# Optimization experiments

Measured on AMD Instinct MI355X. Metric: run time of the kernel, lower is better.

## Reference

```python
import jax, jax.numpy as jnp
import numpy as np

HOPS = 3
VOCAB, EMBD, STORY_LEN, SENT_LEN, BATCH, QLEN = 50000, 128, 200, 32, 64, 32
INIT_RNG = 0.1


def setup_inputs() -> dict:
    key = jax.random.key(0)
    k1, k2, k3, k4, k5 = jax.random.split(key, 5)
    x = jax.random.randint(k1, (BATCH, STORY_LEN, SENT_LEN), 0, VOCAB)          # story token ids
    q = jax.random.randint(k2, (BATCH, QLEN), 0, VOCAB)                          # question token ids
    # hops+1 embedding tables, initialized ~ Normal(mean=-0.1, std=0.1) as in the torch code
    A = jax.random.normal(k3, (HOPS + 1, VOCAB, EMBD), dtype=jnp.float32) * INIT_RNG - INIT_RNG
    TA = jax.random.normal(k4, (STORY_LEN,), dtype=jnp.float32) * INIT_RNG - INIT_RNG
    TC = jax.random.normal(k5, (STORY_LEN,), dtype=jnp.float32) * INIT_RNG - INIT_RNG
    return {"A": A, "TA": TA, "TC": TC, "x": x, "q": q}


def reference(A, TA, TC, x, q):
    # dropout p=0.0 -> identity
    # u: question embedding, summed over query tokens -> [B, E]
    u = jnp.take(A[1], q, axis=0).sum(axis=1)
    for k in range(HOPS):
        # memory (m) and output (c) representations: gather + sum over sentence tokens + temporal encoding
        m = jnp.take(A[k], x, axis=0).sum(axis=2) + TA[None, :, None]      # [B, S, E]
        c = jnp.take(A[k + 1], x, axis=0).sum(axis=2) + TC[None, :, None]  # [B, S, E]
        p = jax.nn.softmax(jnp.einsum("bse,be->bs", m, u), axis=-1)        # attention over story [B, S]
        u = jnp.einsum("bse,bs->be", c, p) + u                              # weighted combine + residual
    logits = u @ A[HOPS].T                                                  # W = A[-1].weight.T -> [B, V]
    return jax.nn.log_softmax(logits, axis=-1)
```

## Files before the change

### kernel.cpp

```cpp
#include <hip/hip_runtime.h>
#include <math.h>

#define VOCAB 50000
#define EMBD  128
#define SLEN  200
#define TOK   32
#define BATCH 64
#define QLEN  32
#define NSENT (BATCH*SLEN)
#define NTASK (4*NSENT + BATCH)
#define TBL   ((size_t)VOCAB*EMBD)
#define NTILE 3125

typedef short short8 __attribute__((ext_vector_type(8)));
typedef float f32x4  __attribute__((ext_vector_type(4)));

__device__ inline float bits2f(unsigned u){ union{unsigned u; float f;}c; c.u=u; return c.f; }
__device__ inline unsigned f2bits(float f){ union{float f; unsigned u;}c; c.f=f; return c.u; }
__device__ inline unsigned pack_bf16(float lo, float hi){
    unsigned ul = f2bits(lo), uh = f2bits(hi);
    unsigned rl = (ul + 0x7fffu + ((ul>>16)&1u)) >> 16;
    unsigned rh = (uh + 0x7fffu + ((uh>>16)&1u)) >> 16;
    return rl | (rh<<16);
}
__device__ inline unsigned short bf16of(float f){
    unsigned u = f2bits(f);
    return (unsigned short)((u + 0x7fffu + ((u>>16)&1u)) >> 16);
}

__device__ inline float waveSum(float v) {
    #pragma unroll
    for (int o = 32; o > 0; o >>= 1) v += __shfl_down(v, o, 64);
    return v;
}
__device__ inline float waveMax(float v) {
    #pragma unroll
    for (int o = 32; o > 0; o >>= 1) v = fmaxf(v, __shfl_down(v, o, 64));
    return v;
}

__global__ __launch_bounds__(256) void conv_kernel(
    const float* __restrict__ A, unsigned* __restrict__ Ab)
{
    size_t i = ((size_t)blockIdx.x*256 + threadIdx.x)*8;
    float4 a = *(const float4*)(A+i);
    float4 b = *(const float4*)(A+i+4);
    uint4 o;
    o.x = pack_bf16(a.x,a.y); o.y = pack_bf16(a.z,a.w);
    o.z = pack_bf16(b.x,b.y); o.w = pack_bf16(b.z,b.w);
    *(uint4*)(Ab + i/2) = o;
}

__global__ __launch_bounds__(256) void gather_kernel(
    const unsigned* __restrict__ Ab, const int* __restrict__ x,
    const int* __restrict__ q, float* __restrict__ G, float* __restrict__ uF)
{
    int B = blockIdx.x;
    int wid = threadIdx.x >> 6;
    int w;
    if (B < 12800) {
        int k = (B & 7) >> 1;
        int i = (B >> 3)*2 + (B & 1);
        w = k*NSENT + i*4 + wid;
    } else {
        w = B*4 + wid;
    }
    int lane = threadIdx.x & 63;
    const int*      idxp;
    const unsigned* tbl;
    bool qtask = (w >= 4*NSENT);
    float* outp;
    if (!qtask) {
        int k  = w / NSENT;
        int bs = w - k * NSENT;
        idxp = x + (size_t)bs * TOK;
        tbl  = Ab + (size_t)k * (TBL/2);
        outp = G + (size_t)w * EMBD;
    } else {
        int b = w - 4 * NSENT;
        idxp = q + (size_t)b * QLEN;
        tbl  = Ab + (TBL/2);
        outp = uF + (size_t)b * EMBD;
    }
    int tg = lane >> 4;
    int sl = lane & 15;
    int idxs[8];
    #pragma unroll
    for (int i = 0; i < 8; i++) idxs[i] = idxp[i*4 + tg];
    float acc[8];
    #pragma unroll
    for (int c = 0; c < 8; c++) acc[c] = 0.f;
    #pragma unroll
    for (int i = 0; i < 8; i++) {
        uint4 v = *(const uint4*)(tbl + (size_t)idxs[i]*64 + sl*4);
        acc[0] += bits2f(v.x<<16); acc[1] += bits2f(v.x&0xffff0000u);
        acc[2] += bits2f(v.y<<16); acc[3] += bits2f(v.y&0xffff0000u);
        acc[4] += bits2f(v.z<<16); acc[5] += bits2f(v.z&0xffff0000u);
        acc[6] += bits2f(v.w<<16); acc[7] += bits2f(v.w&0xffff0000u);
    }
    #pragma unroll
    for (int c = 0; c < 8; c++) {
        acc[c] += __shfl_xor(acc[c], 32, 64);
        acc[c] += __shfl_xor(acc[c], 16, 64);
    }
    if (lane < 32) {
        int g = lane & 15, h = lane >> 4;
        float4 r; r.x = acc[4*h]; r.y = acc[4*h+1]; r.z = acc[4*h+2]; r.w = acc[4*h+3];
        ((float4*)outp)[2*g + h] = r;
    }
}

__global__ __launch_bounds__(1024) void hops_kernel(
    const float* __restrict__ G, const float* __restrict__ uF,
    const float* __restrict__ TA, const float* __restrict__ TC,
    unsigned short* __restrict__ ub)
{
    int b = blockIdx.x;
    int t = threadIdx.x;
    int lane = t & 63, wid = t >> 6;
    __shared__ __align__(16) float Gs[SLEN*132];
    __shared__ __align__(16) float uL[EMBD];
    __shared__ float p[256];
    __shared__ float red[16], red2[16];
    __shared__ float pc[7*EMBD];

    if (t < EMBD) uL[t] = uF[(size_t)b * EMBD + t];
    __syncthreads();

    for (int k = 0; k < 3; k++) {
        float v = (t < EMBD) ? uL[t] : 0.f;
        v = waveSum(v);
        if (lane == 0) red[wid] = v;
        __syncthreads();
        float sumU = 0.f;
        #pragma unroll
        for (int i = 0; i < 16; i++) sumU += red[i];
        int s = t >> 2, qd = t & 3;
        if (s < SLEN) {
            const float4* u4 = (const float4*)uL;
            float dot = 0.f;
            if (k == 0) {
                const float4* g4 = (const float4*)(G + ((size_t)b*SLEN + s)*EMBD);
                #pragma unroll
                for (int e = 0; e < 8; e++) {
                    float4 gg = g4[qd*8+e], uu = u4[qd*8+e];
                    dot += gg.x*uu.x + gg.y*uu.y + gg.z*uu.z + gg.w*uu.w;
                }
            } else {
                const float4* g4 = (const float4*)(Gs + s*132);
                #pragma unroll
                for (int e = 0; e < 8; e++) {
                    float4 gg = g4[qd*8+e], uu = u4[qd*8+e];
                    dot += gg.x*uu.x + gg.y*uu.y + gg.z*uu.z + gg.w*uu.w;
                }
            }
            dot += __shfl_xor(dot, 1, 64);
            dot += __shfl_xor(dot, 2, 64);
            if (qd == 0) p[s] = dot + TA[s]*sumU;
        }
        __syncthreads();
        float mv = (t < SLEN) ? p[t] : -3.4e38f;
        mv = waveMax(mv);
        if (lane == 0) red[wid] = mv;
        __syncthreads();
        float M = -3.4e38f;
        #pragma unroll
        for (int i = 0; i < 16; i++) M = fmaxf(M, red[i]);
        __syncthreads();
        float ev = 0.f, tc = 0.f;
        if (t < SLEN) { ev = __expf(p[t] - M); p[t] = ev; tc = ev * TC[t]; }
        float sv = waveSum(ev);
        float tv = waveSum(tc);
        if (lane == 0) { red[wid] = sv; red2[wid] = tv; }
        __syncthreads();
        float sumP = 0.f, pTC = 0.f;
        #pragma unroll
        for (int i = 0; i < 16; i++) { sumP += red[i]; pTC += red2[i]; }
        const float* Gc = G + ((size_t)(k+1)*NSENT + (size_t)b*SLEN)*EMBD;
        int e = t & 127, ch = t >> 7;
        float acc = 0.f;
        for (int s2 = ch*25; s2 < ch*25 + 25; s2++) {
            float g = Gc[(size_t)s2*EMBD + e];
            Gs[s2*132 + e] = g;
            acc += p[s2] * g;
        }
        if (ch > 0) pc[(ch-1)*EMBD + e] = acc;
        __syncthreads();
        if (ch == 0) {
            #pragma unroll
            for (int c = 0; c < 7; c++) acc += pc[c*EMBD + e];
            uL[e] += (acc + pTC) / sumP;
        }
        __syncthreads();
    }
    if (t < EMBD) ub[(size_t)b * EMBD + t] = bf16of(uL[t]);
}

__global__ __launch_bounds__(256) void logits_mfma(
    const unsigned short* __restrict__ A3b, const unsigned short* __restrict__ ub,
    float* __restrict__ out, float* __restrict__ part)
{
    int w = blockIdx.x*4 + (threadIdx.x >> 6);
    if (w >= NTILE) return;
    int lane = threadIdx.x & 63;
    int col = lane & 15, quad = lane >> 4;
    int v0 = w * 16;

    short8 af[4][4];
    #pragma unroll
    for (int bt = 0; bt < 4; bt++)
        #pragma unroll
        for (int kc = 0; kc < 4; kc++)
            af[bt][kc] = *(const short8*)(ub + (bt*16 + col)*EMBD + kc*32 + quad*8);

    f32x4 acc[4];
    #pragma unroll
    for (int bt = 0; bt < 4; bt++) acc[bt] = (f32x4){0.f, 0.f, 0.f, 0.f};

    #pragma unroll
    for (int kc = 0; kc < 4; kc++) {
        short8 bf = *(const short8*)(A3b + (size_t)(v0 + col)*EMBD + kc*32 + quad*8);
        #pragma unroll
        for (int bt = 0; bt < 4; bt++)
            acc[bt] = __builtin_amdgcn_mfma_f32_16x16x32_bf16(af[bt][kc], bf, acc[bt], 0, 0, 0);
    }

    #pragma unroll
    for (int bt = 0; bt < 4; bt++) {
        #pragma unroll
        for (int r = 0; r < 4; r++) {
            int bI = bt*16 + quad*4 + r;
            out[(size_t)bI * VOCAB + v0 + col] = acc[bt][r];
        }
        #pragma unroll
        for (int r = 0; r < 4; r++) {
            float m = acc[bt][r];
            #pragma unroll
            for (int o = 1; o < 16; o <<= 1) m = fmaxf(m, __shfl_xor(m, o, 64));
            float se = __expf(acc[bt][r] - m);
            #pragma unroll
            for (int o = 1; o < 16; o <<= 1) se += __shfl_xor(se, o, 64);
            if (col == 0) {
                int bI = bt*16 + quad*4 + r;
                float2 pr; pr.x = m; pr.y = se;
                ((float2*)part)[(size_t)bI * NTILE + w] = pr;
            }
        }
    }
}

__global__ __launch_bounds__(256) void norm_kernel(
    float* __restrict__ out, const float* __restrict__ part)
{
    int b = blockIdx.x / 49, c = blockIdx.x % 49;
    int t = threadIdx.x, lane = t & 63, wid = t >> 6;
    __shared__ float sm[4], sl[4];
    const float2* P = (const float2*)part + (size_t)b * NTILE;
    float M = -3.4e38f, L = 0.f;
    for (int i = t; i < NTILE; i += 256) {
        float2 pr = P[i];
        float m2 = fmaxf(M, pr.x);
        L = L * __expf(M - m2) + pr.y * __expf(pr.x - m2);
        M = m2;
    }
    #pragma unroll
    for (int o = 1; o < 64; o <<= 1) {
        float Mo = __shfl_xor(M, o, 64), Lo = __shfl_xor(L, o, 64);
        float m2 = fmaxf(M, Mo);
        L = L * __expf(M - m2) + Lo * __expf(Mo - m2);
        M = m2;
    }
    if (lane == 0) { sm[wid] = M; sl[wid] = L; }
    __syncthreads();
    float Mf = -3.4e38f, Lf = 0.f;
    #pragma unroll
    for (int i = 0; i < 4; i++) {
        float m2 = fmaxf(Mf, sm[i]);
        Lf = Lf * __expf(Mf - m2) + sl[i] * __expf(sm[i] - m2);
        Mf = m2;
    }
    float lse = Mf + __logf(Lf);
    int f4 = c * 256 + t;
    if (f4 < VOCAB/4) {
        float4* rowp = (float4*)(out + (size_t)b * VOCAB);
        float4 v = rowp[f4];
        v.x -= lse; v.y -= lse; v.z -= lse; v.w -= lse;
        rowp[f4] = v;
    }
}

extern "C" void kernel_launch(void* const* d_in, const int* in_sizes, int n_in,
                              void* d_out, int out_size, void* d_ws, size_t ws_size,
                              hipStream_t stream)
{
    const float* A  = (const float*)d_in[0];
    const float* TA = (const float*)d_in[1];
    const float* TC = (const float*)d_in[2];
    const int*   x  = (const int*)d_in[3];
    const int*   q  = (const int*)d_in[4];
    float* out = (float*)d_out;

    unsigned* Ab = (unsigned*)d_ws;
    float* G   = (float*)((char*)d_ws + (size_t)4*TBL*2);
    float* uF  = G + (size_t)4*NSENT*EMBD;
    unsigned short* ubp = (unsigned short*)(uF + (size_t)BATCH*EMBD);
    float* part = (float*)(ubp + (size_t)BATCH*EMBD);

    conv_kernel  <<<12500, 256, 0, stream>>>(A, Ab);
    gather_kernel<<<NTASK/4, 256, 0, stream>>>(Ab, x, q, G, uF);
    hops_kernel  <<<BATCH, 1024, 0, stream>>>(G, uF, TA, TC, ubp);
    logits_mfma  <<<(NTILE+3)/4, 256, 0, stream>>>(
        (const unsigned short*)Ab + (size_t)3*TBL, ubp, out, part);
    norm_kernel  <<<BATCH*49, 256, 0, stream>>>(out, part);
}
```

Before: 277.7 us.

## Interleave four bf16 tables per vocab row so one gather serves all hops

The conversion kernel now writes the four embedding tables interleaved per vocabulary row, 16-element chunks of each table side by side. The gather kernel reads one contiguous 128-byte chunk per token covering all four tables, so each token row is fetched once instead of four times from scattered tables. Nontemporal loads and stores are added for the streaming G buffer and the source table, and the logits kernel reads A3 through the new layout. This trades contiguous per-table rows in the logits kernel for strided 16-byte pieces, and uses more shuffle reductions per wave in the gather.

```diff
diff --git a/kernel.cpp b/kernel.cpp
--- a/kernel.cpp
+++ b/kernel.cpp
@@ -8,12 +8,13 @@
 #define BATCH 64
 #define QLEN  32
 #define NSENT (BATCH*SLEN)
-#define NTASK (4*NSENT + BATCH)
 #define TBL   ((size_t)VOCAB*EMBD)
 #define NTILE 3125
+#define GMAIN 25600
 
 typedef short short8 __attribute__((ext_vector_type(8)));
 typedef float f32x4  __attribute__((ext_vector_type(4)));
+typedef unsigned u32x4 __attribute__((ext_vector_type(4)));
 
 __device__ inline float bits2f(unsigned u){ union{unsigned u; float f;}c; c.u=u; return c.f; }
 __device__ inline unsigned f2bits(float f){ union{float f; unsigned u;}c; c.f=f; return c.u; }
@@ -40,73 +41,99 @@
 }
 
 __global__ __launch_bounds__(256) void conv_kernel(
-    const float* __restrict__ A, unsigned* __restrict__ Ab)
-{
-    size_t i = ((size_t)blockIdx.x*256 + threadIdx.x)*8;
-    float4 a = *(const float4*)(A+i);
-    float4 b = *(const float4*)(A+i+4);
-    uint4 o;
-    o.x = pack_bf16(a.x,a.y); o.y = pack_bf16(a.z,a.w);
-    o.z = pack_bf16(b.x,b.y); o.w = pack_bf16(b.z,b.w);
-    *(uint4*)(Ab + i/2) = o;
+    const float* __restrict__ A, unsigned* __restrict__ Ab2)
+{
+    int id = blockIdx.x*256 + threadIdx.x;
+    if (id >= VOCAB*8) return;
+    int v = id >> 3, c = id & 7;
+    unsigned* dst = Ab2 + (size_t)v*256 + c*32;
+    #pragma unroll
+    for (int k = 0; k < 4; k++) {
+        const f32x4* src = (const f32x4*)(A + (size_t)k*TBL + (size_t)v*EMBD + c*16);
+        f32x4 a = __builtin_nontemporal_load(src);
+        f32x4 b = __builtin_nontemporal_load(src+1);
+        f32x4 d = __builtin_nontemporal_load(src+2);
+        f32x4 e = __builtin_nontemporal_load(src+3);
+        u32x4 o1, o2;
+        o1.x = pack_bf16(a.x,a.y); o1.y = pack_bf16(a.z,a.w);
+        o1.z = pack_bf16(b.x,b.y); o1.w = pack_bf16(b.z,b.w);
+        o2.x = pack_bf16(d.x,d.y); o2.y = pack_bf16(d.z,d.w);
+        o2.z = pack_bf16(e.x,e.y); o2.w = pack_bf16(e.z,e.w);
+        *(u32x4*)(dst + k*8)     = o1;
+        *(u32x4*)(dst + k*8 + 4) = o2;
+    }
 }
 
 __global__ __launch_bounds__(256) void gather_kernel(
-    const unsigned* __restrict__ Ab, const int* __restrict__ x,
+    const unsigned* __restrict__ Ab2, const int* __restrict__ x,
     const int* __restrict__ q, float* __restrict__ G, float* __restrict__ uF)
 {
     int B = blockIdx.x;
-    int wid = threadIdx.x >> 6;
-    int w;
-    if (B < 12800) {
-        int k = (B & 7) >> 1;
-        int i = (B >> 3)*2 + (B & 1);
-        w = k*NSENT + i*4 + wid;
+    int wid = threadIdx.x >> 6, lane = threadIdx.x & 63;
+    if (B < GMAIN) {
+        int c  = B & 7;
+        int bs = (B >> 3)*4 + wid;
+        int tok8 = lane >> 3, sub8 = lane & 7;
+        int k = sub8 >> 1, half = sub8 & 1;
+        const int* idxp = x + (size_t)bs * TOK;
+        float a0=0.f,a1=0.f,a2=0.f,a3=0.f,a4=0.f,a5=0.f,a6=0.f,a7=0.f;
+        #pragma unroll
+        for (int r = 0; r < 4; r++) {
+            int idx = idxp[r*8 + tok8];
+            u32x4 v = *(const u32x4*)(Ab2 + (size_t)idx*256 + c*32 + k*8 + half*4);
+            a0 += bits2f(v.x<<16); a1 += bits2f(v.x&0xffff0000u);
+            a2 += bits2f(v.y<<16); a3 += bits2f(v.y&0xffff0000u);
+            a4 += bits2f(v.z<<16); a5 += bits2f(v.z&0xffff0000u);
+            a6 += bits2f(v.w<<16); a7 += bits2f(v.w&0xffff0000u);
+        }
+        #pragma unroll
+        for (int o = 8; o <= 32; o <<= 1) {
+            a0 += __shfl_xor(a0,o,64); a1 += __shfl_xor(a1,o,64);
+            a2 += __shfl_xor(a2,o,64); a3 += __shfl_xor(a3,o,64);
+            a4 += __shfl_xor(a4,o,64); a5 += __shfl_xor(a5,o,64);
+            a6 += __shfl_xor(a6,o,64); a7 += __shfl_xor(a7,o,64);
+        }
+        if (tok8 < 2) {
+            f32x4 rr;
+            if (tok8 == 0) { rr.x=a0; rr.y=a1; rr.z=a2; rr.w=a3; }
+            else           { rr.x=a4; rr.y=a5; rr.z=a6; rr.w=a7; }
+            float* dst = G + ((size_t)k*NSENT + bs)*EMBD + c*16 + half*8 + tok8*4;
+            __builtin_nontemporal_store(rr, (f32x4*)dst);
+        }
     } else {
-        w = B*4 + wid;
-    }
-    int lane = threadIdx.x & 63;
-    const int*      idxp;
-    const unsigned* tbl;
-    bool qtask = (w >= 4*NSENT);
-    float* outp;
-    if (!qtask) {
-        int k  = w / NSENT;
-        int bs = w - k * NSENT;
-        idxp = x + (size_t)bs * TOK;
-        tbl  = Ab + (size_t)k * (TBL/2);
-        outp = G + (size_t)w * EMBD;
-    } else {
-        int b = w - 4 * NSENT;
-        idxp = q + (size_t)b * QLEN;
-        tbl  = Ab + (TBL/2);
-        outp = uF + (size_t)b * EMBD;
-    }
-    int tg = lane >> 4;
-    int sl = lane & 15;
-    int idxs[8];
-    #pragma unroll
-    for (int i = 0; i < 8; i++) idxs[i] = idxp[i*4 + tg];
-    float acc[8];
-    #pragma unroll
-    for (int c = 0; c < 8; c++) acc[c] = 0.f;
-    #pragma unroll
-    for (int i = 0; i < 8; i++) {
-        uint4 v = *(const uint4*)(tbl + (size_t)idxs[i]*64 + sl*4);
-        acc[0] += bits2f(v.x<<16); acc[1] += bits2f(v.x&0xffff0000u);
-        acc[2] += bits2f(v.y<<16); acc[3] += bits2f(v.y&0xffff0000u);
-        acc[4] += bits2f(v.z<<16); acc[5] += bits2f(v.z&0xffff0000u);
-        acc[6] += bits2f(v.w<<16); acc[7] += bits2f(v.w&0xffff0000u);
-    }
-    #pragma unroll
-    for (int c = 0; c < 8; c++) {
-        acc[c] += __shfl_xor(acc[c], 32, 64);
-        acc[c] += __shfl_xor(acc[c], 16, 64);
-    }
-    if (lane < 32) {
-        int g = lane & 15, h = lane >> 4;
-        float4 r; r.x = acc[4*h]; r.y = acc[4*h+1]; r.z = acc[4*h+2]; r.w = acc[4*h+3];
-        ((float4*)outp)[2*g + h] = r;
+        int b = (B - GMAIN)*4 + wid;
+        int tok8 = lane >> 3, c = lane & 7;
+        const int* idxp = q + (size_t)b * QLEN;
+        float ac[16];
+        #pragma unroll
+        for (int i = 0; i < 16; i++) ac[i] = 0.f;
+        #pragma unroll
+        for (int r = 0; r < 4; r++) {
+            int idx = idxp[r*8 + tok8];
+            const unsigned* base = Ab2 + (size_t)idx*256 + c*32 + 8;
+            u32x4 v1 = *(const u32x4*)base;
+            u32x4 v2 = *(const u32x4*)(base + 4);
+            ac[0] += bits2f(v1.x<<16); ac[1] += bits2f(v1.x&0xffff0000u);
+            ac[2] += bits2f(v1.y<<16); ac[3] += bits2f(v1.y&0xffff0000u);
+            ac[4] += bits2f(v1.z<<16); ac[5] += bits2f(v1.z&0xffff0000u);
+            ac[6] += bits2f(v1.w<<16); ac[7] += bits2f(v1.w&0xffff0000u);
+            ac[8] += bits2f(v2.x<<16); ac[9] += bits2f(v2.x&0xffff0000u);
+            ac[10]+= bits2f(v2.y<<16); ac[11]+= bits2f(v2.y&0xffff0000u);
+            ac[12]+= bits2f(v2.z<<16); ac[13]+= bits2f(v2.z&0xffff0000u);
+            ac[14]+= bits2f(v2.w<<16); ac[15]+= bits2f(v2.w&0xffff0000u);
+        }
+        #pragma unroll
+        for (int o = 8; o <= 32; o <<= 1)
+            #pragma unroll
+            for (int i = 0; i < 16; i++) ac[i] += __shfl_xor(ac[i],o,64);
+        if (tok8 < 4) {
+            f32x4 rr;
+            if      (tok8 == 0) { rr.x=ac[0];  rr.y=ac[1];  rr.z=ac[2];  rr.w=ac[3];  }
+            else if (tok8 == 1) { rr.x=ac[4];  rr.y=ac[5];  rr.z=ac[6];  rr.w=ac[7];  }
+            else if (tok8 == 2) { rr.x=ac[8];  rr.y=ac[9];  rr.z=ac[10]; rr.w=ac[11]; }
+            else                { rr.x=ac[12]; rr.y=ac[13]; rr.z=ac[14]; rr.w=ac[15]; }
+            *(f32x4*)(uF + (size_t)b*EMBD + c*16 + tok8*4) = rr;
+        }
     }
 }
 
@@ -140,10 +167,11 @@
             const float4* u4 = (const float4*)uL;
             float dot = 0.f;
             if (k == 0) {
-                const float4* g4 = (const float4*)(G + ((size_t)b*SLEN + s)*EMBD);
+                const f32x4* g4 = (const f32x4*)(G + ((size_t)b*SLEN + s)*EMBD);
                 #pragma unroll
                 for (int e = 0; e < 8; e++) {
-                    float4 gg = g4[qd*8+e], uu = u4[qd*8+e];
+                    f32x4 gg = __builtin_nontemporal_load(g4 + qd*8 + e);
+                    float4 uu = u4[qd*8+e];
                     dot += gg.x*uu.x + gg.y*uu.y + gg.z*uu.z + gg.w*uu.w;
                 }
             } else {
@@ -180,7 +208,7 @@
         int e = t & 127, ch = t >> 7;
         float acc = 0.f;
         for (int s2 = ch*25; s2 < ch*25 + 25; s2++) {
-            float g = Gc[(size_t)s2*EMBD + e];
+            float g = __builtin_nontemporal_load(Gc + (size_t)s2*EMBD + e);
             Gs[s2*132 + e] = g;
             acc += p[s2] * g;
         }
@@ -197,7 +225,7 @@
 }
 
 __global__ __launch_bounds__(256) void logits_mfma(
-    const unsigned short* __restrict__ A3b, const unsigned short* __restrict__ ub,
+    const unsigned* __restrict__ Ab2, const unsigned short* __restrict__ ub,
     float* __restrict__ out, float* __restrict__ part)
 {
     int w = blockIdx.x*4 + (threadIdx.x >> 6);
@@ -219,7 +247,10 @@
 
     #pragma unroll
     for (int kc = 0; kc < 4; kc++) {
-        short8 bf = *(const short8*)(A3b + (size_t)(v0 + col)*EMBD + kc*32 + quad*8);
+        int c = kc*2 + (quad>>1);
+        const u32x4* bp = (const u32x4*)(Ab2 + (size_t)(v0+col)*256 + c*32 + 24 + (quad&1)*4);
+        u32x4 braw = __builtin_nontemporal_load(bp);
+        short8 bf = *(short8*)&braw;
         #pragma unroll
         for (int bt = 0; bt < 4; bt++)
             acc[bt] = __builtin_amdgcn_mfma_f32_16x16x32_bf16(af[bt][kc], bf, acc[bt], 0, 0, 0);
@@ -300,16 +331,15 @@
     const int*   q  = (const int*)d_in[4];
     float* out = (float*)d_out;
 
-    unsigned* Ab = (unsigned*)d_ws;
+    unsigned* Ab2 = (unsigned*)d_ws;
     float* G   = (float*)((char*)d_ws + (size_t)4*TBL*2);
     float* uF  = G + (size_t)4*NSENT*EMBD;
     unsigned short* ubp = (unsigned short*)(uF + (size_t)BATCH*EMBD);
     float* part = (float*)(ubp + (size_t)BATCH*EMBD);
 
-    conv_kernel  <<<12500, 256, 0, stream>>>(A, Ab);
-    gather_kernel<<<NTASK/4, 256, 0, stream>>>(Ab, x, q, G, uF);
+    conv_kernel  <<<(VOCAB*8 + 255)/256, 256, 0, stream>>>(A, Ab2);
+    gather_kernel<<<GMAIN + 16, 256, 0, stream>>>(Ab2, x, q, G, uF);
     hops_kernel  <<<BATCH, 1024, 0, stream>>>(G, uF, TA, TC, ubp);
-    logits_mfma  <<<(NTILE+3)/4, 256, 0, stream>>>(
-        (const unsigned short*)Ab + (size_t)3*TBL, ubp, out, part);
+    logits_mfma  <<<(NTILE+3)/4, 256, 0, stream>>>(Ab2, ubp, out, part);
     norm_kernel  <<<BATCH*49, 256, 0, stream>>>(out, part);
 }
```

After: 307.8 us. 10.8% more time.
